# Kernel optimization log

Measured on AMD Instinct MI355X. Metric: run time of the kernel, lower is better.

Reference implementation:

```python
import jax, jax.numpy as jnp
import numpy as np

H = 23            # hidden size
NUM_LAYERS = 3
F_IN = 32         # input features
OUT = 8           # output size
B = 2048
T = 512


def _gru_dir(x_seq, w_ih, w_hh, b_ih, b_hh, reverse):
    """One direction of a GRU layer. x_seq: [T,B,in] -> [T,B,H] (time-aligned)."""
    # Precompute input-side gates for all timesteps: [T,B,3H]
    xg = jnp.einsum('tbi,gi->tbg', x_seq, w_ih) + b_ih

    def step(h, xg_t):
        hg = h @ w_hh.T + b_hh                      # [B,3H]
        r = jax.nn.sigmoid(xg_t[:, :H] + hg[:, :H])
        z = jax.nn.sigmoid(xg_t[:, H:2 * H] + hg[:, H:2 * H])
        n = jnp.tanh(xg_t[:, 2 * H:] + r * hg[:, 2 * H:])
        h_new = (1.0 - z) * n + z * h
        return h_new, h_new

    h0 = jnp.zeros((x_seq.shape[1], H), x_seq.dtype)
    _, ys = jax.lax.scan(step, h0, xg, reverse=reverse)
    return ys  # outputs aligned to original time order for both directions


def setup_inputs() -> dict:
    key = jax.random.key(0)
    ks = jax.random.split(key, 16)
    s = 1.0 / np.sqrt(H)  # PyTorch GRU default init scale

    def u(k, shape):
        return jax.random.uniform(k, shape, jnp.float32, -s, s)

    inp = {}
    inp['x'] = jax.random.normal(ks[0], (B, T, F_IN), jnp.float32)
    inp['feature_mean'] = jax.random.normal(ks[1], (F_IN,), jnp.float32) * 0.1
    # std in (0.5, 1.5): no zeros, no exact ones
    inp['feature_std'] = jax.random.uniform(ks[2], (F_IN,), jnp.float32, 0.5, 1.5)
    inp['output_mean'] = jax.random.normal(ks[3], (OUT,), jnp.float32) * 0.1
    inp['output_std'] = jax.random.uniform(ks[4], (OUT,), jnp.float32, 0.5, 1.5)

    # layer 0 params, stacked over direction [2, ...]
    inp['w_ih_l0'] = u(ks[5], (2, 3 * H, F_IN))
    inp['w_hh_l0'] = u(ks[6], (2, 3 * H, H))
    inp['b_ih_l0'] = u(ks[7], (2, 3 * H))
    inp['b_hh_l0'] = u(ks[8], (2, 3 * H))
    # layers 1..2, input size = 2H; stacked [layer, dir, ...]
    inp['w_ih_rest'] = u(ks[9], (NUM_LAYERS - 1, 2, 3 * H, 2 * H))
    inp['w_hh_rest'] = u(ks[10], (NUM_LAYERS - 1, 2, 3 * H, H))
    inp['b_ih_rest'] = u(ks[11], (NUM_LAYERS - 1, 2, 3 * H))
    inp['b_hh_rest'] = u(ks[12], (NUM_LAYERS - 1, 2, 3 * H))

    # fc: xavier_uniform for weight, pytorch default uniform for bias
    fan = OUT + 2 * H
    lim = np.sqrt(6.0 / fan)
    inp['fc_w'] = jax.random.uniform(ks[13], (OUT, 2 * H), jnp.float32, -lim, lim)
    bl = 1.0 / np.sqrt(2 * H)
    inp['fc_b'] = jax.random.uniform(ks[14], (OUT,), jnp.float32, -bl, bl)
    return inp


def reference(x, feature_mean, feature_std, output_mean, output_std,
              w_ih_l0, w_hh_l0, b_ih_l0, b_hh_l0,
              w_ih_rest, w_hh_rest, b_ih_rest, b_hh_rest,
              fc_w, fc_b):
    # feature normalization: std==0 -> 1, then zero out features where adjusted std==1
    std_adj = jnp.where(feature_std == 0.0, 1.0, feature_std)
    x = jnp.where(std_adj == 1.0, 0.0, (x - feature_mean) / std_adj)

    seq = jnp.swapaxes(x, 0, 1)  # [T,B,F] for scan over time
    for layer in range(NUM_LAYERS):
        if layer == 0:
            wih, whh, bih, bhh = w_ih_l0, w_hh_l0, b_ih_l0, b_hh_l0
        else:
            wih, whh = w_ih_rest[layer - 1], w_hh_rest[layer - 1]
            bih, bhh = b_ih_rest[layer - 1], b_hh_rest[layer - 1]
        fwd = _gru_dir(seq, wih[0], whh[0], bih[0], bhh[0], reverse=False)
        bwd = _gru_dir(seq, wih[1], whh[1], bih[1], bhh[1], reverse=True)
        seq = jnp.concatenate([fwd, bwd], axis=-1)  # [T,B,2H]

    last = seq[-1]                 # out[:, -1, :] in batch_first layout -> [B,2H]
    out = last @ fc_w.T + fc_b     # [B,OUT]
    out = out * output_std + output_mean
    return out
```

## Files before the change

kernel.cpp:

```cpp
#include <hip/hip_runtime.h>
#include <hip/hip_bf16.h>

constexpr int TT = 512, BB = 2048, NOUT = 8;
constexpr size_t DSTRIDE = (size_t)BB * TT * 24;

typedef __attribute__((ext_vector_type(8))) short bf16x8;
typedef __attribute__((ext_vector_type(4))) float f32x4;
typedef __attribute__((ext_vector_type(2))) _Float16 f16x2;

__device__ __forceinline__ float sigm(float x) {
    float e = __builtin_amdgcn_exp2f(x * -1.4426950408889634f);
    return __builtin_amdgcn_rcpf(1.f + e);
}
__device__ __forceinline__ float tanh_(float x) {
    float e = __builtin_amdgcn_exp2f(x * 2.8853900817779268f);
    return __builtin_fmaf(-2.f, __builtin_amdgcn_rcpf(e + 1.f), 1.f);
}
__device__ __forceinline__ unsigned short f2bf(float x) {
    __hip_bfloat16 h = __float2bfloat16(x);
    unsigned short s;
    __builtin_memcpy(&s, &h, 2);
    return s;
}
__device__ __forceinline__ f16x2 asf16x2(unsigned v) {
    f16x2 r; __builtin_memcpy(&r, &v, 4); return r;
}
__device__ __forceinline__ void wbar() { __builtin_amdgcn_wave_barrier(); }

template <bool L0, bool LAST>
__global__ __launch_bounds__(256) void gru_mfma(
    const void* __restrict__ in_,
    const float* __restrict__ fmean, const float* __restrict__ fstd,
    const float* __restrict__ wih_g, const float* __restrict__ whh_g,
    const float* __restrict__ bih_g, const float* __restrict__ bhh_g,
    __hip_bfloat16* __restrict__ outbuf, float* __restrict__ lastbuf)
{
    constexpr int KIN = L0 ? 32 : 46;
    constexpr int KF  = L0 ? 1 : 2;

    __shared__ __align__(16) short     wih_lds[5 * 8 * 16 * 8];
    __shared__ __align__(16) _Float16  whh_h[80 * 24];
    __shared__ __align__(16) float     xg_s[4][2][16 * 84];
    __shared__ __align__(16) _Float16  hist_h[4 * 9 * 2 * 32];
    __shared__ float bih_s[80], bhh_s[80];
    __shared__ __align__(16) float an_s[32], cn_s[32];

    const int tid = threadIdx.x, wv = tid >> 6, lane = tid & 63;
    const int bl = lane >> 5, u = lane & 31;
    const int m  = lane & 15, kg = lane >> 4;
    const int dir = blockIdx.y;
    const int bg  = blockIdx.x * 8 + wv * 2 + bl;

    const float* wih_d = wih_g + dir * 69 * KIN;
    const float* whh_d = whh_g + dir * 69 * 23;

    for (int idx = tid; idx < 5120; idx += 256) {
        int t = idx >> 10, r = idx & 1023;
        int kslot = r >> 7, mm = (r >> 3) & 15, j = r & 7;
        int row = t * 16 + mm, k = kslot * 8 + j;
        float v = 0.f;
        if (row < 69) {
            if constexpr (L0) {
                if (k < 32) v = wih_d[row * 32 + k];
            } else {
                if (k < 23) v = wih_d[row * 46 + k];
                else if (k >= 24 && k < 47) v = wih_d[row * 46 + k - 1];
            }
        }
        wih_lds[idx] = (short)f2bf(v);
    }
    for (int idx = tid; idx < 80 * 24; idx += 256) {
        int j = idx / 24, k = idx - j * 24;
        whh_h[idx] = (j < 69 && k < 23) ? (_Float16)whh_d[j * 23 + k]
                                        : (_Float16)0.f;
    }
    for (int idx = tid; idx < 80; idx += 256) {
        bih_s[idx] = (idx < 69) ? bih_g[dir * 69 + idx] : 0.f;
        bhh_s[idx] = (idx < 69) ? bhh_g[dir * 69 + idx] : 0.f;
    }
    for (int idx = tid; idx < 4 * 9 * 2 * 32; idx += 256)
        hist_h[idx] = (_Float16)0.f;
    if (L0 && tid < 32) {
        float sd = fstd[tid];
        float sa = (sd == 0.f) ? 1.f : sd;
        float a  = (sa == 1.f) ? 0.f : 1.f / sa;
        an_s[tid] = a;
        cn_s[tid] = -fmean[tid] * a;
    }
    __syncthreads();

    unsigned wrp[3][12];
    float bh2;
    #pragma unroll
    for (int r = 0; r < 3; ++r) {
        int row = r * 23 + u;
        #pragma unroll
        for (int k = 0; k < 12; ++k)
            wrp[r][k] = *(const unsigned*)&whh_h[row * 24 + 2 * k];
    }
    bh2 = bhh_s[46 + u];
    float bi5[5];
    #pragma unroll
    for (int t = 0; t < 5; ++t) {
        int n = t * 16 + m;
        bi5[t] = bih_s[n] + (n < 46 ? bhh_s[n] : 0.f);
    }

    const bf16x8* bfrag = (const bf16x8*)wih_lds;
    bf16x8 bfr[5][KF];
    #pragma unroll
    for (int t = 0; t < 5; ++t)
        #pragma unroll
        for (int kf = 0; kf < KF; ++kf)
            bfr[t][kf] = bfrag[(t * 8 + kf * 4 + kg) * 16 + m];

    float an8[L0 ? 8 : 1], cn8[L0 ? 8 : 1];
    if constexpr (L0) {
        #pragma unroll
        for (int j = 0; j < 8; ++j) {
            an8[j] = an_s[kg * 8 + j];
            cn8[j] = cn_s[kg * 8 + j];
        }
    }

    float* db0 = &xg_s[wv][0][0];
    float* db1 = &xg_s[wv][1][0];
    _Float16* hw = &hist_h[wv * 9 * 2 * 32];
    const int ngroups = (LAST && dir == 1) ? 1 : 64;
    float hold = 0.f;

    int sarr[3], cparr[3], ldsoff[3];
    {
        int idx = lane & 31;
        #pragma unroll
        for (int c = 0; c < 3; ++c) {
            int p = idx + 32 * c;
            sarr[c]  = p / 12;
            cparr[c] = p - 12 * sarr[c];
            ldsoff[c] = ((sarr[c] + 1) * 2 + bl) * 32 + 2 * cparr[c];
        }
    }
    unsigned short* dstbase = nullptr;
    if constexpr (!LAST)
        dstbase = (unsigned short*)outbuf + dir * DSTRIDE + (size_t)bg * TT * 24;

    const int bl_a = m >> 3, tl = m & 7;
    const int b_a  = blockIdx.x * 8 + wv * 2 + bl_a;

    const unsigned short* r0 = (const unsigned short*)in_;
    const unsigned short* r1 = r0 + DSTRIDE;

    float4 xraw0, xraw1;
    bf16x8 a0r, a1r;

    {
        const int tg_a = dir ? (511 - tl) : tl;
        if constexpr (L0) {
            const float* xr = (const float*)in_ +
                              ((size_t)b_a * TT + tg_a) * 32 + kg * 8;
            xraw0 = *(const float4*)xr;
            xraw1 = *(const float4*)(xr + 4);
        } else {
            size_t rowoff = ((size_t)b_a * TT + tg_a) * 24;
            const unsigned short* p0 =
                (kg < 3) ? (r0 + rowoff + 8 * kg) : (r1 + rowoff);
            const unsigned short* p1 =
                (kg == 0) ? (r1 + rowoff + 8) : (r1 + rowoff + 16);
            a0r = *(const bf16x8*)p0;
            a1r = *(const bf16x8*)p1;
        }
    }

    {
        f32x4 acc[5];
        #pragma unroll
        for (int t = 0; t < 5; ++t)
            acc[t] = (f32x4){bi5[t], bi5[t], bi5[t], bi5[t]};
        if constexpr (L0) {
            float xv[8] = {xraw0.x, xraw0.y, xraw0.z, xraw0.w,
                           xraw1.x, xraw1.y, xraw1.z, xraw1.w};
            bf16x8 afr;
            #pragma unroll
            for (int j = 0; j < 8; ++j)
                afr[j] = (short)f2bf(xv[j] * an8[j] + cn8[j]);
            #pragma unroll
            for (int t = 0; t < 5; ++t)
                acc[t] = __builtin_amdgcn_mfma_f32_16x16x32_bf16(afr, bfr[t][0],
                                                                 acc[t], 0, 0, 0);
        } else {
            bf16x8 a0u = a0r;
            bf16x8 a1u = (kg >= 2) ? (bf16x8){0,0,0,0,0,0,0,0} : a1r;
            #pragma unroll
            for (int t = 0; t < 5; ++t) {
                acc[t] = __builtin_amdgcn_mfma_f32_16x16x32_bf16(a0u, bfr[t][0],
                                                                 acc[t], 0, 0, 0);
                acc[t] = __builtin_amdgcn_mfma_f32_16x16x32_bf16(a1u, bfr[t][1],
                                                                 acc[t], 0, 0, 0);
            }
        }
        #pragma unroll
        for (int t = 0; t < 5; ++t)
            #pragma unroll
            for (int reg = 0; reg < 4; ++reg)
                db0[(kg * 4 + reg) * 84 + t * 16 + m] = acc[t][reg];
    }
    if (1 < ngroups) {
        const int tg_a = dir ? (511 - (8 + tl)) : (8 + tl);
        if constexpr (L0) {
            const float* xr = (const float*)in_ +
                              ((size_t)b_a * TT + tg_a) * 32 + kg * 8;
            xraw0 = *(const float4*)xr;
            xraw1 = *(const float4*)(xr + 4);
        } else {
            size_t rowoff = ((size_t)b_a * TT + tg_a) * 24;
            const unsigned short* p0 =
                (kg < 3) ? (r0 + rowoff + 8 * kg) : (r1 + rowoff);
            const unsigned short* p1 =
                (kg == 0) ? (r1 + rowoff + 8) : (r1 + rowoff + 16);
            a0r = *(const bf16x8*)p0;
            a1r = *(const bf16x8*)p1;
        }
    }

    int cur = 0;
    for (int g = 0; g < ngroups; ++g) {
        float* Dc = cur ? db1 : db0;
        float* Dn = cur ? db0 : db1;
        wbar();

        float xgr[8][3];
        #pragma unroll
        for (int s = 0; s < 8; ++s) {
            const float* xr2 = &Dc[(bl * 8 + s) * 84];
            xgr[s][0] = xr2[u];
            xgr[s][1] = xr2[23 + u];
            xgr[s][2] = xr2[46 + u];
        }

        if (g + 1 < ngroups) {
            f32x4 acc[5];
            #pragma unroll
            for (int t = 0; t < 5; ++t)
                acc[t] = (f32x4){bi5[t], bi5[t], bi5[t], bi5[t]};
            if constexpr (L0) {
                float xv[8] = {xraw0.x, xraw0.y, xraw0.z, xraw0.w,
                               xraw1.x, xraw1.y, xraw1.z, xraw1.w};
                bf16x8 afr;
                #pragma unroll
                for (int j = 0; j < 8; ++j)
                    afr[j] = (short)f2bf(xv[j] * an8[j] + cn8[j]);
                #pragma unroll
                for (int t = 0; t < 5; ++t)
                    acc[t] = __builtin_amdgcn_mfma_f32_16x16x32_bf16(
                        afr, bfr[t][0], acc[t], 0, 0, 0);
            } else {
                bf16x8 a0u = a0r;
                bf16x8 a1u = (kg >= 2) ? (bf16x8){0,0,0,0,0,0,0,0} : a1r;
                #pragma unroll
                for (int t = 0; t < 5; ++t) {
                    acc[t] = __builtin_amdgcn_mfma_f32_16x16x32_bf16(
                        a0u, bfr[t][0], acc[t], 0, 0, 0);
                    acc[t] = __builtin_amdgcn_mfma_f32_16x16x32_bf16(
                        a1u, bfr[t][1], acc[t], 0, 0, 0);
                }
            }
            #pragma unroll
            for (int t = 0; t < 5; ++t)
                #pragma unroll
                for (int reg = 0; reg < 4; ++reg)
                    Dn[(kg * 4 + reg) * 84 + t * 16 + m] = acc[t][reg];

            if (g + 2 < ngroups) {
                const int tg_n = dir ? (511 - ((g + 2) * 8 + tl))
                                     : ((g + 2) * 8 + tl);
                if constexpr (L0) {
                    const float* xr = (const float*)in_ +
                                      ((size_t)b_a * TT + tg_n) * 32 + kg * 8;
                    xraw0 = *(const float4*)xr;
                    xraw1 = *(const float4*)(xr + 4);
                } else {
                    size_t rowoff = ((size_t)b_a * TT + tg_n) * 24;
                    const unsigned short* p0 =
                        (kg < 3) ? (r0 + rowoff + 8 * kg) : (r1 + rowoff);
                    const unsigned short* p1 =
                        (kg == 0) ? (r1 + rowoff + 8) : (r1 + rowoff + 16);
                    a0r = *(const bf16x8*)p0;
                    a1r = *(const bf16x8*)p1;
                }
            }
        }

        #pragma unroll
        for (int s8 = 0; s8 < 8; ++s8) {
            const _Float16* hr = &hw[(s8 * 2 + bl) * 32];
            uint4 hq0 = *(const uint4*)hr;
            uint4 hq1 = *(const uint4*)(hr + 8);
            uint4 hq2 = *(const uint4*)(hr + 16);
            unsigned hwd[12] = {hq0.x, hq0.y, hq0.z, hq0.w,
                                hq1.x, hq1.y, hq1.z, hq1.w,
                                hq2.x, hq2.y, hq2.z, hq2.w};
            float a0a = xgr[s8][0], a1a = xgr[s8][1], a2a = bh2;
            float a0b = 0.f, a1b = 0.f, a2b = 0.f;
            #pragma unroll
            for (int k = 0; k < 6; ++k) {
                f16x2 hv = asf16x2(hwd[k]);
                a0a = __builtin_amdgcn_fdot2(asf16x2(wrp[0][k]), hv, a0a, false);
                a1a = __builtin_amdgcn_fdot2(asf16x2(wrp[1][k]), hv, a1a, false);
                a2a = __builtin_amdgcn_fdot2(asf16x2(wrp[2][k]), hv, a2a, false);
            }
            #pragma unroll
            for (int k = 6; k < 12; ++k) {
                f16x2 hv = asf16x2(hwd[k]);
                a0b = __builtin_amdgcn_fdot2(asf16x2(wrp[0][k]), hv, a0b, false);
                a1b = __builtin_amdgcn_fdot2(asf16x2(wrp[1][k]), hv, a1b, false);
                a2b = __builtin_amdgcn_fdot2(asf16x2(wrp[2][k]), hv, a2b, false);
            }
            float r_ = sigm(a0a + a0b);
            float z_ = sigm(a1a + a1b);
            float n_ = tanh_(__builtin_fmaf(r_, a2a + a2b, xgr[s8][2]));
            float hnew = n_ + z_ * (hold - n_);
            hold = hnew;
            if constexpr (LAST) {
                int tg = dir ? (511 - (g * 8 + s8)) : (g * 8 + s8);
                if (u < 23 && tg == TT - 1)
                    lastbuf[bg * 48 + dir * 23 + u] = hnew;
            }
            wbar();
            hw[((s8 + 1) * 2 + bl) * 32 + u] = (_Float16)hnew;
            wbar();
        }

        if constexpr (!LAST) {
            #pragma unroll
            for (int c = 0; c < 3; ++c) {
                f16x2 pf = asf16x2(*(const unsigned*)&hw[ldsoff[c]]);
                float lo = (float)pf[0];
                float hi = (cparr[c] == 11) ? 0.f : (float)pf[1];
                unsigned pack = (unsigned)f2bf(lo) | ((unsigned)f2bf(hi) << 16);
                int tg = dir ? (511 - (g * 8 + sarr[c])) : (g * 8 + sarr[c]);
                *(unsigned*)(dstbase + (size_t)tg * 24 + 2 * cparr[c]) = pack;
            }
        }
        hw[bl * 32 + u] = (_Float16)hold;
        wbar();
        cur ^= 1;
    }
}

__global__ __launch_bounds__(256) void fc_kernel(
    const float* __restrict__ last, const float* __restrict__ fcw,
    const float* __restrict__ fcb, const float* __restrict__ ostd,
    const float* __restrict__ omean, float* __restrict__ out)
{
    int idx = blockIdx.x * 256 + threadIdx.x;
    if (idx >= BB * NOUT) return;
    int b = idx >> 3, o = idx & 7;
    float acc = fcb[o];
    const float* lr = last + b * 48;
    const float* wr = fcw + o * 46;
    #pragma unroll
    for (int i = 0; i < 46; i++) acc += lr[i] * wr[i];
    out[idx] = acc * ostd[o] + omean[o];
}

extern "C" void kernel_launch(void* const* d_in, const int* in_sizes, int n_in,
                              void* d_out, int out_size, void* d_ws,
                              size_t ws_size, hipStream_t stream)
{
    const float* x     = (const float*)d_in[0];
    const float* fmean = (const float*)d_in[1];
    const float* fstd  = (const float*)d_in[2];
    const float* omean = (const float*)d_in[3];
    const float* ostd  = (const float*)d_in[4];
    const float* wih0  = (const float*)d_in[5];
    const float* whh0  = (const float*)d_in[6];
    const float* bih0  = (const float*)d_in[7];
    const float* bhh0  = (const float*)d_in[8];
    const float* wihr  = (const float*)d_in[9];
    const float* whhr  = (const float*)d_in[10];
    const float* bihr  = (const float*)d_in[11];
    const float* bhhr  = (const float*)d_in[12];
    const float* fcw   = (const float*)d_in[13];
    const float* fcb   = (const float*)d_in[14];

    char* ws = (char*)d_ws;
    const size_t bufBytes = 2 * DSTRIDE * sizeof(__hip_bfloat16);
    __hip_bfloat16* buf0 = (__hip_bfloat16*)ws;
    __hip_bfloat16* buf1 = (__hip_bfloat16*)(ws + bufBytes);
    float* lastb         = (float*)(ws + 2 * bufBytes);

    dim3 grid(BB / 8, 2);

    gru_mfma<true, false><<<grid, 256, 0, stream>>>(
        x, fmean, fstd, wih0, whh0, bih0, bhh0, buf0, nullptr);
    gru_mfma<false, false><<<grid, 256, 0, stream>>>(
        buf0, nullptr, nullptr, wihr + 0 * 2 * 69 * 46, whhr + 0 * 2 * 69 * 23,
        bihr + 0 * 2 * 69, bhhr + 0 * 2 * 69, buf1, nullptr);
    gru_mfma<false, true><<<grid, 256, 0, stream>>>(
        buf1, nullptr, nullptr, wihr + 1 * 2 * 69 * 46, whhr + 1 * 2 * 69 * 23,
        bihr + 1 * 2 * 69, bhhr + 1 * 2 * 69, nullptr, lastb);
    fc_kernel<<<(BB * NOUT + 255) / 256, 256, 0, stream>>>(lastb, fcw, fcb, ostd,
                                                           omean, (float*)d_out);
}
```

Before: 638.0 us.

## Switch input projection and inter-layer buffers from bf16 to fp16, transpose xg LDS layout

Moves the input-gate MFMA from bf16 to fp16. Inter-layer activations are now stored as fp16 straight from the fp16 history buffer, and layer-0 inputs are converted with packed RTZ conversions, so the per-element bf16 conversions in the store and input paths go away. The xg staging buffer in LDS is transposed to gate-major with a stride of 20, so MFMA results are written as f32x4 vectors and read back with two vector loads per gate instead of eight scalar loads. The risk is fp16 range and precision on normalized inputs, and possible LDS bank conflicts from the new stride.

```diff
diff --git a/kernel.cpp b/kernel.cpp
--- a/kernel.cpp
+++ b/kernel.cpp
@@ -4,7 +4,7 @@
 constexpr int TT = 512, BB = 2048, NOUT = 8;
 constexpr size_t DSTRIDE = (size_t)BB * TT * 24;
 
-typedef __attribute__((ext_vector_type(8))) short bf16x8;
+typedef __attribute__((ext_vector_type(8))) _Float16 f16x8;
 typedef __attribute__((ext_vector_type(4))) float f32x4;
 typedef __attribute__((ext_vector_type(2))) _Float16 f16x2;
 
@@ -16,14 +16,12 @@
     float e = __builtin_amdgcn_exp2f(x * 2.8853900817779268f);
     return __builtin_fmaf(-2.f, __builtin_amdgcn_rcpf(e + 1.f), 1.f);
 }
-__device__ __forceinline__ unsigned short f2bf(float x) {
-    __hip_bfloat16 h = __float2bfloat16(x);
-    unsigned short s;
-    __builtin_memcpy(&s, &h, 2);
-    return s;
-}
 __device__ __forceinline__ f16x2 asf16x2(unsigned v) {
     f16x2 r; __builtin_memcpy(&r, &v, 4); return r;
+}
+__device__ __forceinline__ f16x2 pkrtz(float a, float b) {
+    auto p = __builtin_amdgcn_cvt_pkrtz(a, b);
+    f16x2 r; __builtin_memcpy(&r, &p, 4); return r;
 }
 __device__ __forceinline__ void wbar() { __builtin_amdgcn_wave_barrier(); }
 
@@ -33,14 +31,15 @@
     const float* __restrict__ fmean, const float* __restrict__ fstd,
     const float* __restrict__ wih_g, const float* __restrict__ whh_g,
     const float* __restrict__ bih_g, const float* __restrict__ bhh_g,
-    __hip_bfloat16* __restrict__ outbuf, float* __restrict__ lastbuf)
+    unsigned short* __restrict__ outbuf, float* __restrict__ lastbuf)
 {
     constexpr int KIN = L0 ? 32 : 46;
     constexpr int KF  = L0 ? 1 : 2;
-
-    __shared__ __align__(16) short     wih_lds[5 * 8 * 16 * 8];
+    constexpr int DSTR = 20;
+
+    __shared__ __align__(16) _Float16  wih_lds[5 * 8 * 16 * 8];
     __shared__ __align__(16) _Float16  whh_h[80 * 24];
-    __shared__ __align__(16) float     xg_s[4][2][16 * 84];
+    __shared__ __align__(16) float     xg_s[4][2][80 * DSTR];
     __shared__ __align__(16) _Float16  hist_h[4 * 9 * 2 * 32];
     __shared__ float bih_s[80], bhh_s[80];
     __shared__ __align__(16) float an_s[32], cn_s[32];
@@ -67,7 +66,7 @@
                 else if (k >= 24 && k < 47) v = wih_d[row * 46 + k - 1];
             }
         }
-        wih_lds[idx] = (short)f2bf(v);
+        wih_lds[idx] = (_Float16)v;
     }
     for (int idx = tid; idx < 80 * 24; idx += 256) {
         int j = idx / 24, k = idx - j * 24;
@@ -106,8 +105,8 @@
         bi5[t] = bih_s[n] + (n < 46 ? bhh_s[n] : 0.f);
     }
 
-    const bf16x8* bfrag = (const bf16x8*)wih_lds;
-    bf16x8 bfr[5][KF];
+    const f16x8* bfrag = (const f16x8*)wih_lds;
+    f16x8 bfr[5][KF];
     #pragma unroll
     for (int t = 0; t < 5; ++t)
         #pragma unroll
@@ -142,7 +141,7 @@
     }
     unsigned short* dstbase = nullptr;
     if constexpr (!LAST)
-        dstbase = (unsigned short*)outbuf + dir * DSTRIDE + (size_t)bg * TT * 24;
+        dstbase = outbuf + dir * DSTRIDE + (size_t)bg * TT * 24;
 
     const int bl_a = m >> 3, tl = m & 7;
     const int b_a  = blockIdx.x * 8 + wv * 2 + bl_a;
@@ -151,7 +150,7 @@
     const unsigned short* r1 = r0 + DSTRIDE;
 
     float4 xraw0, xraw1;
-    bf16x8 a0r, a1r;
+    f16x8 a0r, a1r;
 
     {
         const int tg_a = dir ? (511 - tl) : tl;
@@ -166,8 +165,8 @@
                 (kg < 3) ? (r0 + rowoff + 8 * kg) : (r1 + rowoff);
             const unsigned short* p1 =
                 (kg == 0) ? (r1 + rowoff + 8) : (r1 + rowoff + 16);
-            a0r = *(const bf16x8*)p0;
-            a1r = *(const bf16x8*)p1;
+            a0r = *(const f16x8*)p0;
+            a1r = *(const f16x8*)p1;
         }
     }
 
@@ -179,30 +178,33 @@
         if constexpr (L0) {
             float xv[8] = {xraw0.x, xraw0.y, xraw0.z, xraw0.w,
                            xraw1.x, xraw1.y, xraw1.z, xraw1.w};
-            bf16x8 afr;
-            #pragma unroll
-            for (int j = 0; j < 8; ++j)
-                afr[j] = (short)f2bf(xv[j] * an8[j] + cn8[j]);
+            f16x8 afr;
+            #pragma unroll
+            for (int j = 0; j < 4; ++j) {
+                f16x2 p = pkrtz(xv[2 * j] * an8[2 * j] + cn8[2 * j],
+                                xv[2 * j + 1] * an8[2 * j + 1] + cn8[2 * j + 1]);
+                afr[2 * j]     = p[0];
+                afr[2 * j + 1] = p[1];
+            }
             #pragma unroll
             for (int t = 0; t < 5; ++t)
-                acc[t] = __builtin_amdgcn_mfma_f32_16x16x32_bf16(afr, bfr[t][0],
-                                                                 acc[t], 0, 0, 0);
+                acc[t] = __builtin_amdgcn_mfma_f32_16x16x32_f16(afr, bfr[t][0],
+                                                                acc[t], 0, 0, 0);
         } else {
-            bf16x8 a0u = a0r;
-            bf16x8 a1u = (kg >= 2) ? (bf16x8){0,0,0,0,0,0,0,0} : a1r;
+            f16x8 zz = {};
+            f16x8 a0u = a0r;
+            f16x8 a1u = (kg >= 2) ? zz : a1r;
             #pragma unroll
             for (int t = 0; t < 5; ++t) {
-                acc[t] = __builtin_amdgcn_mfma_f32_16x16x32_bf16(a0u, bfr[t][0],
-                                                                 acc[t], 0, 0, 0);
-                acc[t] = __builtin_amdgcn_mfma_f32_16x16x32_bf16(a1u, bfr[t][1],
-                                                                 acc[t], 0, 0, 0);
+                acc[t] = __builtin_amdgcn_mfma_f32_16x16x32_f16(a0u, bfr[t][0],
+                                                                acc[t], 0, 0, 0);
+                acc[t] = __builtin_amdgcn_mfma_f32_16x16x32_f16(a1u, bfr[t][1],
+                                                                acc[t], 0, 0, 0);
             }
         }
         #pragma unroll
         for (int t = 0; t < 5; ++t)
-            #pragma unroll
-            for (int reg = 0; reg < 4; ++reg)
-                db0[(kg * 4 + reg) * 84 + t * 16 + m] = acc[t][reg];
+            *(f32x4*)&db0[(t * 16 + m) * DSTR + kg * 4] = acc[t];
     }
     if (1 < ngroups) {
         const int tg_a = dir ? (511 - (8 + tl)) : (8 + tl);
@@ -217,8 +219,8 @@
                 (kg < 3) ? (r0 + rowoff + 8 * kg) : (r1 + rowoff);
             const unsigned short* p1 =
                 (kg == 0) ? (r1 + rowoff + 8) : (r1 + rowoff + 16);
-            a0r = *(const bf16x8*)p0;
-            a1r = *(const bf16x8*)p1;
+            a0r = *(const f16x8*)p0;
+            a1r = *(const f16x8*)p1;
         }
     }
 
@@ -230,11 +232,12 @@
 
         float xgr[8][3];
         #pragma unroll
-        for (int s = 0; s < 8; ++s) {
-            const float* xr2 = &Dc[(bl * 8 + s) * 84];
-            xgr[s][0] = xr2[u];
-            xgr[s][1] = xr2[23 + u];
-            xgr[s][2] = xr2[46 + u];
+        for (int c = 0; c < 3; ++c) {
+            const f32x4 lo = *(const f32x4*)&Dc[(c * 23 + u) * DSTR + bl * 8];
+            const f32x4 hi = *(const f32x4*)&Dc[(c * 23 + u) * DSTR + bl * 8 + 4];
+            #pragma unroll
+            for (int s = 0; s < 8; ++s)
+                xgr[s][c] = (s < 4) ? lo[s] : hi[s - 4];
         }
 
         if (g + 1 < ngroups) {
@@ -245,30 +248,34 @@
             if constexpr (L0) {
                 float xv[8] = {xraw0.x, xraw0.y, xraw0.z, xraw0.w,
                                xraw1.x, xraw1.y, xraw1.z, xraw1.w};
-                bf16x8 afr;
+                f16x8 afr;
                 #pragma unroll
-                for (int j = 0; j < 8; ++j)
-                    afr[j] = (short)f2bf(xv[j] * an8[j] + cn8[j]);
+                for (int j = 0; j < 4; ++j) {
+                    f16x2 p = pkrtz(
+                        xv[2 * j] * an8[2 * j] + cn8[2 * j],
+                        xv[2 * j + 1] * an8[2 * j + 1] + cn8[2 * j + 1]);
+                    afr[2 * j]     = p[0];
+                    afr[2 * j + 1] = p[1];
+                }
                 #pragma unroll
                 for (int t = 0; t < 5; ++t)
-                    acc[t] = __builtin_amdgcn_mfma_f32_16x16x32_bf16(
+                    acc[t] = __builtin_amdgcn_mfma_f32_16x16x32_f16(
                         afr, bfr[t][0], acc[t], 0, 0, 0);
             } else {
-                bf16x8 a0u = a0r;
-                bf16x8 a1u = (kg >= 2) ? (bf16x8){0,0,0,0,0,0,0,0} : a1r;
+                f16x8 zz = {};
+                f16x8 a0u = a0r;
+                f16x8 a1u = (kg >= 2) ? zz : a1r;
                 #pragma unroll
                 for (int t = 0; t < 5; ++t) {
-                    acc[t] = __builtin_amdgcn_mfma_f32_16x16x32_bf16(
+                    acc[t] = __builtin_amdgcn_mfma_f32_16x16x32_f16(
                         a0u, bfr[t][0], acc[t], 0, 0, 0);
-                    acc[t] = __builtin_amdgcn_mfma_f32_16x16x32_bf16(
+                    acc[t] = __builtin_amdgcn_mfma_f32_16x16x32_f16(
                         a1u, bfr[t][1], acc[t], 0, 0, 0);
                 }
             }
             #pragma unroll
             for (int t = 0; t < 5; ++t)
-                #pragma unroll
-                for (int reg = 0; reg < 4; ++reg)
-                    Dn[(kg * 4 + reg) * 84 + t * 16 + m] = acc[t][reg];
+                *(f32x4*)&Dn[(t * 16 + m) * DSTR + kg * 4] = acc[t];
 
             if (g + 2 < ngroups) {
                 const int tg_n = dir ? (511 - ((g + 2) * 8 + tl))
@@ -284,8 +291,8 @@
                         (kg < 3) ? (r0 + rowoff + 8 * kg) : (r1 + rowoff);
                     const unsigned short* p1 =
                         (kg == 0) ? (r1 + rowoff + 8) : (r1 + rowoff + 16);
-                    a0r = *(const bf16x8*)p0;
-                    a1r = *(const bf16x8*)p1;
+                    a0r = *(const f16x8*)p0;
+                    a1r = *(const f16x8*)p1;
                 }
             }
         }
@@ -333,12 +340,10 @@
         if constexpr (!LAST) {
             #pragma unroll
             for (int c = 0; c < 3; ++c) {
-                f16x2 pf = asf16x2(*(const unsigned*)&hw[ldsoff[c]]);
-                float lo = (float)pf[0];
-                float hi = (cparr[c] == 11) ? 0.f : (float)pf[1];
-                unsigned pack = (unsigned)f2bf(lo) | ((unsigned)f2bf(hi) << 16);
+                unsigned w = *(const unsigned*)&hw[ldsoff[c]];
+                if (cparr[c] == 11) w &= 0xFFFFu;
                 int tg = dir ? (511 - (g * 8 + sarr[c])) : (g * 8 + sarr[c]);
-                *(unsigned*)(dstbase + (size_t)tg * 24 + 2 * cparr[c]) = pack;
+                *(unsigned*)(dstbase + (size_t)tg * 24 + 2 * cparr[c]) = w;
             }
         }
         hw[bl * 32 + u] = (_Float16)hold;
@@ -384,9 +389,9 @@
     const float* fcb   = (const float*)d_in[14];
 
     char* ws = (char*)d_ws;
-    const size_t bufBytes = 2 * DSTRIDE * sizeof(__hip_bfloat16);
-    __hip_bfloat16* buf0 = (__hip_bfloat16*)ws;
-    __hip_bfloat16* buf1 = (__hip_bfloat16*)(ws + bufBytes);
+    const size_t bufBytes = 2 * DSTRIDE * sizeof(unsigned short);
+    unsigned short* buf0 = (unsigned short*)ws;
+    unsigned short* buf1 = (unsigned short*)(ws + bufBytes);
     float* lastb         = (float*)(ws + 2 * bufBytes);
 
     dim3 grid(BB / 8, 2);
```

After: 626.0 us. About the same (-1.9%).
